# Kernel tuning notes

Measured on AMD Instinct MI355X. Metric: run time of the kernel, lower is better.

## Reference

```python
import jax, jax.numpy as jnp
import numpy as np
from jax import lax

BZ, CAP, SEQ, INV = 32, 134, 144, 16
E_SP, E_FT = 1072, 64


def sage(x, e_src, e_dst, Wl, bl, Wr, n_nodes):
    # PyG SAGEConv (mean aggr): out = lin_l(mean_{j->i} x_j) + lin_r(x_i)
    # x: [B, N, F]; edges broadcast over batch
    msgs = x[:, e_src]                                   # [B, E, F] gather
    agg = jnp.zeros_like(x).at[:, e_dst].add(msgs)        # [B, N, F] scatter-add
    deg = jnp.zeros((n_nodes,), x.dtype).at[e_dst].add(1.0)
    mean = agg / jnp.clip(deg, 1.0)[None, :, None]
    return mean @ Wl + bl + x @ Wr


def setup_inputs() -> dict:
    key = jax.random.key(0)
    ks = jax.random.split(key, 16)
    s = lambda fan: 1.0 / np.sqrt(fan)
    inp = {
        'src': jax.random.normal(ks[0], (BZ, CAP, SEQ, INV), jnp.float32),
        'graph_edge_index': jax.random.randint(ks[1], (2, E_SP), 0, CAP, jnp.int32),
        'feature_edge_index': jax.random.randint(ks[2], (2, E_FT), 0, INV, jnp.int32),
        # spatial SAGEConv(in_var, in_var)
        'gcn_Wl': jax.random.uniform(ks[3], (INV, INV), jnp.float32, -s(INV), s(INV)),
        'gcn_bl': jnp.zeros((INV,), jnp.float32),
        'gcn_Wr': jax.random.uniform(ks[4], (INV, INV), jnp.float32, -s(INV), s(INV)),
        # feature SAGEConv(seq_len, seq_len)
        'fgcn_Wl': jax.random.uniform(ks[5], (SEQ, SEQ), jnp.float32, -s(SEQ), s(SEQ)),
        'fgcn_bl': jnp.zeros((SEQ,), jnp.float32),
        'fgcn_Wr': jax.random.uniform(ks[6], (SEQ, SEQ), jnp.float32, -s(SEQ), s(SEQ)),
        # Conv1d(in_var, in_var, k=3/5, no bias): OIW layout
        'conv1_w': jax.random.uniform(ks[7], (INV, INV, 3), jnp.float32, -s(INV * 3), s(INV * 3)),
        'conv2_w': jax.random.uniform(ks[8], (INV, INV, 5), jnp.float32, -s(INV * 5), s(INV * 5)),
        # Linear(3*in_var, in_var)
        'fc_w': jax.random.uniform(ks[9], (3 * INV, INV), jnp.float32, -s(3 * INV), s(3 * INV)),
        'fc_b': jnp.zeros((INV,), jnp.float32),
    }
    return inp


def reference(src, graph_edge_index, feature_edge_index, gcn_Wl, gcn_bl, gcn_Wr,
              fgcn_Wl, fgcn_bl, fgcn_Wr, conv1_w, conv2_w, fc_w, fc_b):
    bz, cap, seq, inv = src.shape
    # --- spatial GCN: nodes = turbines, features = in_var, batched over bz*seq
    x1 = src.transpose(0, 2, 1, 3).reshape(bz * seq, cap, inv)
    sp = sage(x1, graph_edge_index[0], graph_edge_index[1], gcn_Wl, gcn_bl, gcn_Wr, cap)
    spatial_fea = sp.reshape(bz, seq, cap, inv).transpose(0, 2, 1, 3)
    # --- feature GCN: nodes = variables, features = seq_len, batched over bz*cap
    x2 = src.transpose(0, 1, 3, 2).reshape(bz * cap, inv, seq)
    ft = sage(x2, feature_edge_index[0], feature_edge_index[1], fgcn_Wl, fgcn_bl, fgcn_Wr, inv)
    fea_fea = ft.reshape(bz, cap, inv, seq).transpose(0, 1, 3, 2)
    # --- temporal dual Conv1d over seq axis, channels = in_var
    x3 = src.reshape(bz * cap, seq, inv).transpose(0, 2, 1)  # [N, C, L]
    dn = ('NCH', 'OIH', 'NCH')
    c1 = lax.conv_general_dilated(x3, conv1_w, (1,), [(1, 1)], dimension_numbers=dn)
    c2 = lax.conv_general_dilated(x3, conv2_w, (1,), [(2, 2)], dimension_numbers=dn)
    temporal_fea = (c1 + c2).transpose(0, 2, 1).reshape(bz, cap, seq, inv)
    # --- concat + FC fusion + residual (dropout = identity at eval)
    com = jnp.concatenate([spatial_fea, fea_fea, temporal_fea], axis=-1)  # [..., 3*inv]
    out = com @ fc_w + fc_b
    return src + out
```

## Files before the change

### kernel.cpp

```cpp
#include <hip/hip_runtime.h>
#include <hip/hip_bf16.h>

#define BZn 32
#define CAPn 134
#define SEQn 144
#define INVn 16
#define ESP 1072
#define EFT 64


typedef __attribute__((ext_vector_type(8))) short bf16x8;
typedef __attribute__((ext_vector_type(4))) short short4v;
typedef __attribute__((ext_vector_type(4))) float f32x4;

#define MFMA(a, b, c) __builtin_amdgcn_mfma_f32_16x16x32_bf16(a, b, c, 0, 0, 0)

__device__ __forceinline__ unsigned short f2bf(float f) {
    union { float f; unsigned u; } v; v.f = f;
    unsigned r = v.u + 0x7fff + ((v.u >> 16) & 1);
    return (unsigned short)(r >> 16);
}
__device__ __forceinline__ float bf2f(unsigned short h) {
    union { unsigned u; float f; } v; v.u = ((unsigned)h) << 16;
    return v.f;
}
__device__ __forceinline__ unsigned pk2(float a, float b) {
    float2 v; v.x = a; v.y = b;
    union { __hip_bfloat162 h; unsigned u; } c;
    c.h = __float22bfloat162_rn(v);
    return c.u;
}
__device__ __forceinline__ short4v pack4(f32x4 v) {
    union { unsigned u[2]; short4v s; } r;
    r.u[0] = pk2(v[0], v[1]);
    r.u[1] = pk2(v[2], v[3]);
    return r.s;
}

__global__ __launch_bounds__(256) void prep_kernel(
    const int* __restrict__ ge, const int* __restrict__ fe,
    const float* __restrict__ Wl,  const float* __restrict__ Wr,
    const float* __restrict__ fWl, const float* __restrict__ fWr,
    const float* __restrict__ w1,  const float* __restrict__ w2,
    const float* __restrict__ fcw, const float* __restrict__ bl,
    const float* __restrict__ fcb,
    int* __restrict__ ws)
{
    int t = threadIdx.x;
    char* wsb = (char*)ws;
    unsigned short* uB     = (unsigned short*)(wsb + 5376);
    unsigned short* vB     = (unsigned short*)(wsb + 6400);
    unsigned short* spB2   = (unsigned short*)(wsb + 7424);
    float*          biasf  = (float*)(wsb + 8448);
    unsigned short* convA2 = (unsigned short*)(wsb + 8704);
    unsigned short* featB  = (unsigned short*)(wsb + 12800);

    if (blockIdx.x == 0) {
        int* g_rp  = ws;
        int* g_col = ws + 135;
        float* g_inv = (float*)(ws + 1207);
        __shared__ float swt[3360];
        __shared__ int cnt[CAPn], off[CAPn], fm[256];
        __shared__ float finv[16];

        for (int u = t; u < 768;  u += 256) swt[u]        = fcw[u];
        for (int u = t; u < 768;  u += 256) swt[768 + u]  = w1[u];
        for (int u = t; u < 1280; u += 256) swt[1536 + u] = w2[u];
        if (t < 256) swt[2816 + t] = Wl[t];
        if (t < 256) swt[3072 + t] = Wr[t];
        if (t < 16) swt[3328 + t] = bl[t];
        if (t < 16) swt[3344 + t] = fcb[t];

        for (int c0 = t; c0 < CAPn; c0 += 256) cnt[c0] = 0;
        fm[t] = 0;
        __syncthreads();
        for (int e = t; e < ESP; e += 256) atomicAdd(&cnt[ge[ESP + e]], 1);
        if (t < EFT) atomicAdd(&fm[fe[t] * 16 + fe[EFT + t]], 1);
        __syncthreads();
        if (t == 0) {
            int run = 0;
            for (int c0 = 0; c0 < CAPn; c0++) {
                off[c0] = run; g_rp[c0] = run;
                g_inv[c0] = 1.0f / fmaxf((float)cnt[c0], 1.0f);
                run += cnt[c0];
            }
            g_rp[CAPn] = run;
        }
        if (t < 16) {
            int dg = 0;
            for (int j = 0; j < 16; j++) dg += fm[j * 16 + t];
            finv[t] = 1.0f / fmaxf((float)dg, 1.0f);
        }
        __syncthreads();
        for (int c0 = t; c0 < CAPn; c0 += 256) cnt[c0] = 0;
        __syncthreads();
        for (int e = t; e < ESP; e += 256) {
            int d = ge[ESP + e];
            int p = off[d] + atomicAdd(&cnt[d], 1);
            g_col[p] = ge[e];
        }
        for (int u = t; u < 512; u += 256) {
            int l = u >> 3, j = u & 7, k = (l >> 4) * 8 + j, ip = l & 15;
            float vu = 0.f, vv = 0.f, vs = 0.f;
            if (k < 16) {
                for (int i = 0; i < 16; i++)
                    vu += (float)fm[k * 16 + i] * finv[i] * swt[(16 + i) * 16 + ip];
                vv = swt[(16 + k) * 16 + ip];
                for (int i = 0; i < 16; i++) vs += swt[2816 + k * 16 + i] * swt[i * 16 + ip];
            } else {
                for (int i = 0; i < 16; i++) vs += swt[3072 + (k - 16) * 16 + i] * swt[i * 16 + ip];
            }
            uB[u] = f2bf(vu); vB[u] = f2bf(vv); spB2[u] = f2bf(vs);
        }
        for (int u = t; u < 2048; u += 256) {
            int kk2 = u >> 9, l = (u >> 3) & 63, j = u & 7, q = l >> 4, o = l & 15;
            int kkp = kk2 * 2 + (q >> 1), i = (q & 1) * 8 + j;
            float v = 0.f;
            for (int o0 = 0; o0 < 16; o0++) {
                float w = (kkp < 3) ? swt[768 + (o0 * 16 + i) * 3 + kkp]
                                    : swt[1536 + (o0 * 16 + i) * 5 + (kkp - 3)];
                v += w * swt[(32 + o0) * 16 + o];
            }
            convA2[u] = f2bf(v);
        }
        if (t < 16) {
            float b0 = swt[3344 + t], c0 = 0.f;
            for (int i = 0; i < 16; i++) {
                b0 += swt[3328 + i] * swt[i * 16 + t];
                c0 += swt[(16 + i) * 16 + t];
            }
            biasf[t] = b0; biasf[16 + t] = c0;
        }
    } else {
        __shared__ float wtile[32][145];
        int kk = blockIdx.x - 1;
        for (int u = t; u < 32 * 144; u += 256) {
            int r = u / 144, s = u - r * 144;
            int k = kk * 32 + r;
            wtile[r][s] = (k < 144) ? fWl[k * 144 + s] : fWr[(k - 144) * 144 + s];
        }
        __syncthreads();
        for (int u = t; u < 4608; u += 256) {
            int n0 = u >> 9, rem = u & 511;
            int l = rem >> 3, j = rem & 7;
            featB[(kk * 9 + n0) * 512 + rem] =
                f2bf(wtile[(l >> 4) * 8 + j][n0 * 16 + (l & 15)]);
        }
    }
}

__global__ __launch_bounds__(256, 4) void fused_kernel(
    const float* __restrict__ src,
    const float* __restrict__ fbl,
    const int* __restrict__ ws,
    float* __restrict__ out)
{
    const int* g_rp  = ws;
    const int* g_col = ws + 135;
    const float* g_inv = (const float*)(ws + 1207);
    const char* wsb = (const char*)ws;
    const unsigned short* uB     = (const unsigned short*)(wsb + 5376);
    const unsigned short* vB     = (const unsigned short*)(wsb + 6400);
    const unsigned short* spB2   = (const unsigned short*)(wsb + 7424);
    const float*          biasf  = (const float*)(wsb + 8448);
    const unsigned short* convA2 = (const unsigned short*)(wsb + 8704);
    const unsigned short* featB  = (const unsigned short*)(wsb + 12800);

    __shared__ __align__(16) unsigned short xs_bf[SEQn + 4][24];
    __shared__ __align__(16) unsigned short mt_bf[SEQn][24];
    __shared__ __align__(16) unsigned short uv_bf[INVn][312];
    __shared__ float sfbl[SEQn], sbias[16], scs[16];

    int t = threadIdx.x;
    int wave = t >> 6, lane = t & 63;
    int q = lane >> 4, ln = lane & 15;

    int ust_w = (wave == 0) ? 0 : (2 * wave + 1);
    int sst_w = 2 * wave;

    int xcd  = blockIdx.x & 7;
    int slot = blockIdx.x >> 3;
    int bl_  = slot / 134;
    int c    = slot - bl_ * 134;
    int b    = xcd * 4 + bl_;
    int bc   = b * CAPn + c;
    const float* srcb = src + (size_t)b * (CAPn * SEQn * INVn);
    const float* srcc = srcb + (size_t)c * (SEQn * INVn);

    const f32x4* s4 = (const f32x4*)srcc;
    f32x4 x0 = s4[t], x1 = s4[t + 256];
    f32x4 x2 = {0.f,0.f,0.f,0.f};
    if (t < 64) x2 = s4[t + 512];

    int rs = g_rp[c], re = g_rp[c + 1];
    float idg = g_inv[c];
    f32x4 m0a = {0.f,0.f,0.f,0.f}, m1a = {0.f,0.f,0.f,0.f}, m2a = {0.f,0.f,0.f,0.f};
    f32x4 m0b = {0.f,0.f,0.f,0.f}, m1b = {0.f,0.f,0.f,0.f}, m2b = {0.f,0.f,0.f,0.f};
    int e = rs;
    for (; e + 3 < re; e += 4) {
        int n0_ = g_col[e], n1_ = g_col[e + 1], n2_ = g_col[e + 2], n3_ = g_col[e + 3];
        const f32x4* p0 = (const f32x4*)(srcb + (size_t)n0_ * (SEQn * INVn));
        const f32x4* p1 = (const f32x4*)(srcb + (size_t)n1_ * (SEQn * INVn));
        const f32x4* p2 = (const f32x4*)(srcb + (size_t)n2_ * (SEQn * INVn));
        const f32x4* p3 = (const f32x4*)(srcb + (size_t)n3_ * (SEQn * INVn));
        f32x4 a0 = p0[t],       a1 = p1[t],       a2 = p2[t],       a3 = p3[t];
        f32x4 b0 = p0[t + 256], b1 = p1[t + 256], b2 = p2[t + 256], b3 = p3[t + 256];
        f32x4 c0 = {0.f,0.f,0.f,0.f}, c1 = c0, c2 = c0, c3 = c0;
        if (t < 64) { c0 = p0[t + 512]; c1 = p1[t + 512]; c2 = p2[t + 512]; c3 = p3[t + 512]; }
        m0a += a0; m0b += a1; m1a += b0; m1b += b1;
        m0a += a2; m0b += a3; m1a += b2; m1b += b3;
        if (t < 64) { m2a += c0; m2b += c1; m2a += c2; m2b += c3; }
    }
    for (; e + 1 < re; e += 2) {
        int na = g_col[e], nb = g_col[e + 1];
        const f32x4* pa = (const f32x4*)(srcb + (size_t)na * (SEQn * INVn));
        const f32x4* pb = (const f32x4*)(srcb + (size_t)nb * (SEQn * INVn));
        m0a += pa[t];       m0b += pb[t];
        m1a += pa[t + 256]; m1b += pb[t + 256];
        if (t < 64) { m2a += pa[t + 512]; m2b += pb[t + 512]; }
    }
    if (e < re) {
        int na = g_col[e];
        const f32x4* pa = (const f32x4*)(srcb + (size_t)na * (SEQn * INVn));
        m0a += pa[t]; m1a += pa[t + 256];
        if (t < 64) m2a += pa[t + 512];
    }

    bf16x8 caf0 = *(const bf16x8*)(convA2 + (0 * 64 + lane) * 8);
    bf16x8 caf1 = *(const bf16x8*)(convA2 + (1 * 64 + lane) * 8);
    bf16x8 caf2 = *(const bf16x8*)(convA2 + (2 * 64 + lane) * 8);
    bf16x8 caf3 = *(const bf16x8*)(convA2 + (3 * 64 + lane) * 8);
    bf16x8 sbf = *(const bf16x8*)(spB2 + lane * 8);
    bf16x8 ubf = *(const bf16x8*)(uB + lane * 8);
    bf16x8 vbf = *(const bf16x8*)(vB + lane * 8);

    int s0g = t >> 2, i0g = (t & 3) * 4;
    f32x4 m0 = (m0a + m0b) * idg, m1 = (m1a + m1b) * idg, m2 = (m2a + m2b) * idg;
    *(short4v*)&mt_bf[s0g][i0g]      = pack4(m0);
    *(short4v*)&mt_bf[64 + s0g][i0g] = pack4(m1);
    if (t < 64) *(short4v*)&mt_bf[128 + s0g][i0g] = pack4(m2);

    *(short4v*)&xs_bf[s0g + 2][i0g]      = pack4(x0);
    *(short4v*)&xs_bf[64 + s0g + 2][i0g] = pack4(x1);
    if (t < 64) *(short4v*)&xs_bf[128 + s0g + 2][i0g] = pack4(x2);
    if (t < 64) {
        int r = t >> 4, i = t & 15;
        int row = (r < 2) ? r : 144 + r;
        xs_bf[row][i] = 0;
    }
    if (t < SEQn) sfbl[t] = fbl[t];
    if (t < 16) { sbias[t] = biasf[t]; scs[t] = biasf[16 + t]; }
    __syncthreads();

    #pragma unroll
    for (int tt = 0; tt < 3; tt++) {
        if ((wave == 0) || (tt < 2)) {
            int mt = ust_w + tt;
            int sl = mt * 16 + ln;
            bf16x8 a = {0,0,0,0,0,0,0,0};
            if (q < 2) a = *(const bf16x8*)&xs_bf[sl + 2][q * 8];
            f32x4 au = {0.f,0.f,0.f,0.f}, av = {0.f,0.f,0.f,0.f};
            au = MFMA(a, ubf, au);
            av = MFMA(a, vbf, av);
            *(short4v*)&uv_bf[ln][mt * 16 + q * 4]       = pack4(au);
            *(short4v*)&uv_bf[ln][144 + mt * 16 + q * 4] = pack4(av);
        }
    }
    f32x4 accS0 = {0.f,0.f,0.f,0.f}, accS1 = accS0, accS2 = accS0;
    {
        int sl = (sst_w + 0) * 16 + ln;
        const unsigned short* ap = (q < 2) ? &mt_bf[sl][(q & 1) * 8]
                                           : &xs_bf[sl + 2][(q & 1) * 8];
        accS0 = MFMA(*(const bf16x8*)ap, sbf, accS0);
    }
    {
        int sl = (sst_w + 1) * 16 + ln;
        const unsigned short* ap = (q < 2) ? &mt_bf[sl][(q & 1) * 8]
                                           : &xs_bf[sl + 2][(q & 1) * 8];
        accS1 = MFMA(*(const bf16x8*)ap, sbf, accS1);
    }
    if (wave == 3) {
        int sl = (sst_w + 2) * 16 + ln;
        const unsigned short* ap = (q < 2) ? &mt_bf[sl][(q & 1) * 8]
                                           : &xs_bf[sl + 2][(q & 1) * 8];
        accS2 = MFMA(*(const bf16x8*)ap, sbf, accS2);
    }
    __syncthreads();

    #pragma unroll
    for (int tt = 0; tt < 3; tt++) {
        if ((wave == 0) || (tt < 2)) {
            int n0 = ust_w + tt;
            int sl = n0 * 16 + ln;
            bf16x8 bfrag[9];
            #pragma unroll
            for (int kk = 0; kk < 9; kk++)
                bfrag[kk] = *(const bf16x8*)(featB + ((kk * 9 + n0) * 64 + lane) * 8);
            bf16x8 cb[4];
            #pragma unroll
            for (int kk = 0; kk < 4; kk++) {
                int kkp = kk * 2 + (q >> 1);
                int off = (kkp < 3) ? (kkp - 1) : (kkp - 5);
                cb[kk] = *(const bf16x8*)&xs_bf[sl + 2 + off][(q & 1) * 8];
            }
            f32x4 acc = {0.f,0.f,0.f,0.f};
            acc = MFMA(caf0, cb[0], acc);
            acc = MFMA(caf1, cb[1], acc);
            acc = MFMA(caf2, cb[2], acc);
            acc = MFMA(caf3, cb[3], acc);
            #pragma unroll
            for (int kk = 0; kk < 9; kk++) {
                bf16x8 a = *(const bf16x8*)&uv_bf[ln][kk * 32 + q * 8];
                acc = MFMA(a, bfrag[kk], acc);
            }
            *(short4v*)&mt_bf[sl][q * 4] = pack4(acc);
        }
    }
    __syncthreads();

    float* outb = out + (size_t)bc * (SEQn * INVn);
    {
        int mt = sst_w + 0;
        #pragma unroll
        for (int r = 0; r < 4; r++) {
            int s = mt * 16 + q * 4 + r;
            int idx = s * 16 + ln;
            outb[idx] = accS0[r] + bf2f(mt_bf[s][ln]) + srcc[idx]
                      + sbias[ln] + sfbl[s] * scs[ln];
        }
    }
    {
        int mt = sst_w + 1;
        #pragma unroll
        for (int r = 0; r < 4; r++) {
            int s = mt * 16 + q * 4 + r;
            int idx = s * 16 + ln;
            outb[idx] = accS1[r] + bf2f(mt_bf[s][ln]) + srcc[idx]
                      + sbias[ln] + sfbl[s] * scs[ln];
        }
    }
    if (wave == 3) {
        int mt = sst_w + 2;
        #pragma unroll
        for (int r = 0; r < 4; r++) {
            int s = mt * 16 + q * 4 + r;
            int idx = s * 16 + ln;
            outb[idx] = accS2[r] + bf2f(mt_bf[s][ln]) + srcc[idx]
                      + sbias[ln] + sfbl[s] * scs[ln];
        }
    }
}

extern "C" void kernel_launch(void* const* d_in, const int* in_sizes, int n_in,
                              void* d_out, int out_size, void* d_ws, size_t ws_size,
                              hipStream_t stream)
{
    const float* src = (const float*)d_in[0];
    const int* ge = (const int*)d_in[1];
    const int* fe = (const int*)d_in[2];
    const float* Wl  = (const float*)d_in[3];
    const float* blp = (const float*)d_in[4];
    const float* Wr  = (const float*)d_in[5];
    const float* fWl = (const float*)d_in[6];
    const float* fbl = (const float*)d_in[7];
    const float* fWr = (const float*)d_in[8];
    const float* w1  = (const float*)d_in[9];
    const float* w2  = (const float*)d_in[10];
    const float* fcw = (const float*)d_in[11];
    const float* fcb = (const float*)d_in[12];
    float* out = (float*)d_out;
    int* ws = (int*)d_ws;

    hipLaunchKernelGGL(prep_kernel, dim3(10), dim3(256), 0, stream,
                       ge, fe, Wl, Wr, fWl, fWr, w1, w2, fcw, blp, fcb, ws);
    hipLaunchKernelGGL(fused_kernel, dim3(BZn * CAPn), dim3(256), 0, stream,
                       src, fbl, ws, out);
}
```

Baseline: 161.0 us.

## Split fused kernel into temporal and spatial kernels accumulating through output

Splits the single fused kernel into a temporal/feature kernel that writes its partial result to the output, followed by a spatial kernel that gathers neighbour rows and adds its part into the output. The aim is to cut per-block register and LDS pressure and the barriers, and to let each kernel reach higher occupancy. In exchange it adds a kernel launch, an extra full read and write of the output, and a second read of src.

```diff
diff --git a/kernel.cpp b/kernel.cpp
--- a/kernel.cpp
+++ b/kernel.cpp
@@ -19,10 +19,6 @@
     union { float f; unsigned u; } v; v.f = f;
     unsigned r = v.u + 0x7fff + ((v.u >> 16) & 1);
     return (unsigned short)(r >> 16);
-}
-__device__ __forceinline__ float bf2f(unsigned short h) {
-    union { unsigned u; float f; } v; v.u = ((unsigned)h) << 16;
-    return v.f;
 }
 __device__ __forceinline__ unsigned pk2(float a, float b) {
     float2 v; v.x = a; v.y = b;
@@ -149,9 +145,116 @@
     }
 }
 
-__global__ __launch_bounds__(256, 4) void fused_kernel(
+__global__ __launch_bounds__(256, 4) void temporal_kernel(
     const float* __restrict__ src,
     const float* __restrict__ fbl,
+    const int* __restrict__ ws,
+    float* __restrict__ out)
+{
+    const char* wsb = (const char*)ws;
+    const unsigned short* uB     = (const unsigned short*)(wsb + 5376);
+    const unsigned short* vB     = (const unsigned short*)(wsb + 6400);
+    const float*          biasf  = (const float*)(wsb + 8448);
+    const unsigned short* convA2 = (const unsigned short*)(wsb + 8704);
+    const unsigned short* featB  = (const unsigned short*)(wsb + 12800);
+
+    __shared__ __align__(16) unsigned short xs_bf[SEQn + 4][24];
+    __shared__ __align__(16) unsigned short uv_bf[INVn][312];
+    __shared__ float sfbl[SEQn], sbias[16], scs[16];
+
+    int t = threadIdx.x;
+    int wave = t >> 6, lane = t & 63;
+    int q = lane >> 4, ln = lane & 15;
+    int ust_w = (wave == 0) ? 0 : (2 * wave + 1);
+
+    int xcd  = blockIdx.x & 7;
+    int slot = blockIdx.x >> 3;
+    int bl_  = slot / 134;
+    int c    = slot - bl_ * 134;
+    int b    = xcd * 4 + bl_;
+    int bc   = b * CAPn + c;
+    const float* srcc = src + (size_t)b * (CAPn * SEQn * INVn)
+                            + (size_t)c * (SEQn * INVn);
+
+    const f32x4* s4 = (const f32x4*)srcc;
+    f32x4 x0 = s4[t], x1 = s4[t + 256];
+    f32x4 x2 = {0.f,0.f,0.f,0.f};
+    if (t < 64) x2 = s4[t + 512];
+
+    bf16x8 caf0 = *(const bf16x8*)(convA2 + (0 * 64 + lane) * 8);
+    bf16x8 caf1 = *(const bf16x8*)(convA2 + (1 * 64 + lane) * 8);
+    bf16x8 caf2 = *(const bf16x8*)(convA2 + (2 * 64 + lane) * 8);
+    bf16x8 caf3 = *(const bf16x8*)(convA2 + (3 * 64 + lane) * 8);
+    bf16x8 ubf = *(const bf16x8*)(uB + lane * 8);
+    bf16x8 vbf = *(const bf16x8*)(vB + lane * 8);
+
+    int s0g = t >> 2, i0g = (t & 3) * 4;
+    *(short4v*)&xs_bf[s0g + 2][i0g]      = pack4(x0);
+    *(short4v*)&xs_bf[64 + s0g + 2][i0g] = pack4(x1);
+    if (t < 64) *(short4v*)&xs_bf[128 + s0g + 2][i0g] = pack4(x2);
+    if (t < 64) {
+        int r = t >> 4, i = t & 15;
+        int row = (r < 2) ? r : 144 + r;
+        xs_bf[row][i] = 0;
+    }
+    if (t < SEQn) sfbl[t] = fbl[t];
+    if (t < 16) { sbias[t] = biasf[t]; scs[t] = biasf[16 + t]; }
+    __syncthreads();
+
+    #pragma unroll
+    for (int tt = 0; tt < 3; tt++) {
+        if ((wave == 0) || (tt < 2)) {
+            int mt = ust_w + tt;
+            int sl = mt * 16 + ln;
+            bf16x8 a = {0,0,0,0,0,0,0,0};
+            if (q < 2) a = *(const bf16x8*)&xs_bf[sl + 2][q * 8];
+            f32x4 au = {0.f,0.f,0.f,0.f}, av = {0.f,0.f,0.f,0.f};
+            au = MFMA(a, ubf, au);
+            av = MFMA(a, vbf, av);
+            *(short4v*)&uv_bf[ln][mt * 16 + q * 4]       = pack4(au);
+            *(short4v*)&uv_bf[ln][144 + mt * 16 + q * 4] = pack4(av);
+        }
+    }
+    __syncthreads();
+
+    float* outb = out + (size_t)bc * (SEQn * INVn);
+    f32x4 bias4 = *(const f32x4*)&sbias[q * 4];
+    f32x4 cs4   = *(const f32x4*)&scs[q * 4];
+    #pragma unroll
+    for (int tt = 0; tt < 3; tt++) {
+        if ((wave == 0) || (tt < 2)) {
+            int n0 = ust_w + tt;
+            int sl = n0 * 16 + ln;
+            bf16x8 bfrag[9];
+            #pragma unroll
+            for (int kk = 0; kk < 9; kk++)
+                bfrag[kk] = *(const bf16x8*)(featB + ((kk * 9 + n0) * 64 + lane) * 8);
+            bf16x8 cb[4];
+            #pragma unroll
+            for (int kk = 0; kk < 4; kk++) {
+                int kkp = kk * 2 + (q >> 1);
+                int off = (kkp < 3) ? (kkp - 1) : (kkp - 5);
+                cb[kk] = *(const bf16x8*)&xs_bf[sl + 2 + off][(q & 1) * 8];
+            }
+            f32x4 acc = {0.f,0.f,0.f,0.f};
+            acc = MFMA(caf0, cb[0], acc);
+            acc = MFMA(caf1, cb[1], acc);
+            acc = MFMA(caf2, cb[2], acc);
+            acc = MFMA(caf3, cb[3], acc);
+            #pragma unroll
+            for (int kk = 0; kk < 9; kk++) {
+                bf16x8 a = *(const bf16x8*)&uv_bf[ln][kk * 32 + q * 8];
+                acc = MFMA(a, bfrag[kk], acc);
+            }
+            float fb = sfbl[sl];
+            f32x4 res = acc + bias4 + fb * cs4;
+            *(f32x4*)&outb[sl * 16 + q * 4] = res;
+        }
+    }
+}
+
+__global__ __launch_bounds__(256, 4) void spatial_kernel(
+    const float* __restrict__ src,
     const int* __restrict__ ws,
     float* __restrict__ out)
 {
@@ -159,23 +262,14 @@
     const int* g_col = ws + 135;
     const float* g_inv = (const float*)(ws + 1207);
     const char* wsb = (const char*)ws;
-    const unsigned short* uB     = (const unsigned short*)(wsb + 5376);
-    const unsigned short* vB     = (const unsigned short*)(wsb + 6400);
-    const unsigned short* spB2   = (const unsigned short*)(wsb + 7424);
-    const float*          biasf  = (const float*)(wsb + 8448);
-    const unsigned short* convA2 = (const unsigned short*)(wsb + 8704);
-    const unsigned short* featB  = (const unsigned short*)(wsb + 12800);
-
-    __shared__ __align__(16) unsigned short xs_bf[SEQn + 4][24];
-    __shared__ __align__(16) unsigned short mt_bf[SEQn][24];
-    __shared__ __align__(16) unsigned short uv_bf[INVn][312];
-    __shared__ float sfbl[SEQn], sbias[16], scs[16];
+    const unsigned short* spB2 = (const unsigned short*)(wsb + 7424);
+
+    __shared__ __align__(16) unsigned short xs_bf[SEQn][24];
+    __shared__ __align__(16) unsigned short msp_bf[SEQn][24];
 
     int t = threadIdx.x;
     int wave = t >> 6, lane = t & 63;
     int q = lane >> 4, ln = lane & 15;
-
-    int ust_w = (wave == 0) ? 0 : (2 * wave + 1);
     int sst_w = 2 * wave;
 
     int xcd  = blockIdx.x & 7;
@@ -226,97 +320,38 @@
         if (t < 64) m2a += pa[t + 512];
     }
 
-    bf16x8 caf0 = *(const bf16x8*)(convA2 + (0 * 64 + lane) * 8);
-    bf16x8 caf1 = *(const bf16x8*)(convA2 + (1 * 64 + lane) * 8);
-    bf16x8 caf2 = *(const bf16x8*)(convA2 + (2 * 64 + lane) * 8);
-    bf16x8 caf3 = *(const bf16x8*)(convA2 + (3 * 64 + lane) * 8);
     bf16x8 sbf = *(const bf16x8*)(spB2 + lane * 8);
-    bf16x8 ubf = *(const bf16x8*)(uB + lane * 8);
-    bf16x8 vbf = *(const bf16x8*)(vB + lane * 8);
 
     int s0g = t >> 2, i0g = (t & 3) * 4;
     f32x4 m0 = (m0a + m0b) * idg, m1 = (m1a + m1b) * idg, m2 = (m2a + m2b) * idg;
-    *(short4v*)&mt_bf[s0g][i0g]      = pack4(m0);
-    *(short4v*)&mt_bf[64 + s0g][i0g] = pack4(m1);
-    if (t < 64) *(short4v*)&mt_bf[128 + s0g][i0g] = pack4(m2);
-
-    *(short4v*)&xs_bf[s0g + 2][i0g]      = pack4(x0);
-    *(short4v*)&xs_bf[64 + s0g + 2][i0g] = pack4(x1);
-    if (t < 64) *(short4v*)&xs_bf[128 + s0g + 2][i0g] = pack4(x2);
-    if (t < 64) {
-        int r = t >> 4, i = t & 15;
-        int row = (r < 2) ? r : 144 + r;
-        xs_bf[row][i] = 0;
-    }
-    if (t < SEQn) sfbl[t] = fbl[t];
-    if (t < 16) { sbias[t] = biasf[t]; scs[t] = biasf[16 + t]; }
+    *(short4v*)&msp_bf[s0g][i0g]      = pack4(m0);
+    *(short4v*)&msp_bf[64 + s0g][i0g] = pack4(m1);
+    if (t < 64) *(short4v*)&msp_bf[128 + s0g][i0g] = pack4(m2);
+
+    *(short4v*)&xs_bf[s0g][i0g]      = pack4(x0);
+    *(short4v*)&xs_bf[64 + s0g][i0g] = pack4(x1);
+    if (t < 64) *(short4v*)&xs_bf[128 + s0g][i0g] = pack4(x2);
     __syncthreads();
 
-    #pragma unroll
-    for (int tt = 0; tt < 3; tt++) {
-        if ((wave == 0) || (tt < 2)) {
-            int mt = ust_w + tt;
-            int sl = mt * 16 + ln;
-            bf16x8 a = {0,0,0,0,0,0,0,0};
-            if (q < 2) a = *(const bf16x8*)&xs_bf[sl + 2][q * 8];
-            f32x4 au = {0.f,0.f,0.f,0.f}, av = {0.f,0.f,0.f,0.f};
-            au = MFMA(a, ubf, au);
-            av = MFMA(a, vbf, av);
-            *(short4v*)&uv_bf[ln][mt * 16 + q * 4]       = pack4(au);
-            *(short4v*)&uv_bf[ln][144 + mt * 16 + q * 4] = pack4(av);
-        }
-    }
     f32x4 accS0 = {0.f,0.f,0.f,0.f}, accS1 = accS0, accS2 = accS0;
     {
         int sl = (sst_w + 0) * 16 + ln;
-        const unsigned short* ap = (q < 2) ? &mt_bf[sl][(q & 1) * 8]
-                                           : &xs_bf[sl + 2][(q & 1) * 8];
+        const unsigned short* ap = (q < 2) ? &msp_bf[sl][(q & 1) * 8]
+                                           : &xs_bf[sl][(q & 1) * 8];
         accS0 = MFMA(*(const bf16x8*)ap, sbf, accS0);
     }
     {
         int sl = (sst_w + 1) * 16 + ln;
-        const unsigned short* ap = (q < 2) ? &mt_bf[sl][(q & 1) * 8]
-                                           : &xs_bf[sl + 2][(q & 1) * 8];
+        const unsigned short* ap = (q < 2) ? &msp_bf[sl][(q & 1) * 8]
+                                           : &xs_bf[sl][(q & 1) * 8];
         accS1 = MFMA(*(const bf16x8*)ap, sbf, accS1);
     }
     if (wave == 3) {
         int sl = (sst_w + 2) * 16 + ln;
-        const unsigned short* ap = (q < 2) ? &mt_bf[sl][(q & 1) * 8]
-                                           : &xs_bf[sl + 2][(q & 1) * 8];
+        const unsigned short* ap = (q < 2) ? &msp_bf[sl][(q & 1) * 8]
+                                           : &xs_bf[sl][(q & 1) * 8];
         accS2 = MFMA(*(const bf16x8*)ap, sbf, accS2);
     }
-    __syncthreads();
-
-    #pragma unroll
-    for (int tt = 0; tt < 3; tt++) {
-        if ((wave == 0) || (tt < 2)) {
-            int n0 = ust_w + tt;
-            int sl = n0 * 16 + ln;
-            bf16x8 bfrag[9];
-            #pragma unroll
-            for (int kk = 0; kk < 9; kk++)
-                bfrag[kk] = *(const bf16x8*)(featB + ((kk * 9 + n0) * 64 + lane) * 8);
-            bf16x8 cb[4];
-            #pragma unroll
-            for (int kk = 0; kk < 4; kk++) {
-                int kkp = kk * 2 + (q >> 1);
-                int off = (kkp < 3) ? (kkp - 1) : (kkp - 5);
-                cb[kk] = *(const bf16x8*)&xs_bf[sl + 2 + off][(q & 1) * 8];
-            }
-            f32x4 acc = {0.f,0.f,0.f,0.f};
-            acc = MFMA(caf0, cb[0], acc);
-            acc = MFMA(caf1, cb[1], acc);
-            acc = MFMA(caf2, cb[2], acc);
-            acc = MFMA(caf3, cb[3], acc);
-            #pragma unroll
-            for (int kk = 0; kk < 9; kk++) {
-                bf16x8 a = *(const bf16x8*)&uv_bf[ln][kk * 32 + q * 8];
-                acc = MFMA(a, bfrag[kk], acc);
-            }
-            *(short4v*)&mt_bf[sl][q * 4] = pack4(acc);
-        }
-    }
-    __syncthreads();
 
     float* outb = out + (size_t)bc * (SEQn * INVn);
     {
@@ -325,8 +360,7 @@
         for (int r = 0; r < 4; r++) {
             int s = mt * 16 + q * 4 + r;
             int idx = s * 16 + ln;
-            outb[idx] = accS0[r] + bf2f(mt_bf[s][ln]) + srcc[idx]
-                      + sbias[ln] + sfbl[s] * scs[ln];
+            outb[idx] = outb[idx] + accS0[r] + srcc[idx];
         }
     }
     {
@@ -335,8 +369,7 @@
         for (int r = 0; r < 4; r++) {
             int s = mt * 16 + q * 4 + r;
             int idx = s * 16 + ln;
-            outb[idx] = accS1[r] + bf2f(mt_bf[s][ln]) + srcc[idx]
-                      + sbias[ln] + sfbl[s] * scs[ln];
+            outb[idx] = outb[idx] + accS1[r] + srcc[idx];
         }
     }
     if (wave == 3) {
@@ -345,8 +378,7 @@
         for (int r = 0; r < 4; r++) {
             int s = mt * 16 + q * 4 + r;
             int idx = s * 16 + ln;
-            outb[idx] = accS2[r] + bf2f(mt_bf[s][ln]) + srcc[idx]
-                      + sbias[ln] + sfbl[s] * scs[ln];
+            outb[idx] = outb[idx] + accS2[r] + srcc[idx];
         }
     }
 }
@@ -373,6 +405,8 @@
 
     hipLaunchKernelGGL(prep_kernel, dim3(10), dim3(256), 0, stream,
                        ge, fe, Wl, Wr, fWl, fWr, w1, w2, fcw, blp, fcb, ws);
-    hipLaunchKernelGGL(fused_kernel, dim3(BZn * CAPn), dim3(256), 0, stream,
+    hipLaunchKernelGGL(temporal_kernel, dim3(BZn * CAPn), dim3(256), 0, stream,
                        src, fbl, ws, out);
-}
+    hipLaunchKernelGGL(spatial_kernel, dim3(BZn * CAPn), dim3(256), 0, stream,
+                       src, ws, out);
+}
```

New measurement: 173.6 us. 1.08x slower.
